# Kernel tuning notes

Measured on AMD Instinct MI355X. Metric: run time of the kernel, lower is better.

The kernel has to match this reference:

```python
import jax, jax.numpy as jnp
import numpy as np

B, N, E, S, ANN_D, N_STEPS = 16384, 70, 3, 10, 1, 5


def setup_inputs() -> dict:
    key = jax.random.key(0)
    ks = jax.random.split(key, 10)
    std = 0.02
    annotation = jax.random.normal(ks[0], (B, N), jnp.float32)
    A_raw = jax.random.uniform(ks[1], (N, N * E), jnp.float32) + 1e-3
    A = A_raw / A_raw.sum(axis=1, keepdims=True)  # row-normalized like torch.div(A, sum(A,1))
    W_in = jax.random.normal(ks[2], (E, S, S), jnp.float32) * std
    b_in = jnp.zeros((E, S), jnp.float32)
    Wr = jax.random.normal(ks[3], (S, 2 * S), jnp.float32) * std
    br = jnp.zeros((S,), jnp.float32)
    Wz = jax.random.normal(ks[4], (S, 2 * S), jnp.float32) * std
    bz = jnp.zeros((S,), jnp.float32)
    Wh = jax.random.normal(ks[5], (S, 2 * S), jnp.float32) * std
    bh = jnp.zeros((S,), jnp.float32)
    Wo1 = jax.random.normal(ks[6], (S, S + ANN_D), jnp.float32) * std
    bo1 = jnp.zeros((S,), jnp.float32)
    Wo2 = jax.random.normal(ks[7], (1, S), jnp.float32) * std
    bo2 = jnp.zeros((1,), jnp.float32)
    return {"annotation": annotation, "A": A, "W_in": W_in, "b_in": b_in,
            "Wr": Wr, "br": br, "Wz": Wz, "bz": bz, "Wh": Wh, "bh": bh,
            "Wo1": Wo1, "bo1": bo1, "Wo2": Wo2, "bo2": bo2}


def reference(annotation, A, W_in, b_in, Wr, br, Wz, bz, Wh, bh, Wo1, bo1, Wo2, bo2):
    b, n = annotation.shape
    ann = annotation[..., None]  # [B, N, 1]
    # initial state: annotation padded with zeros to state_dim
    prop = jnp.concatenate([ann, jnp.zeros((b, n, S - ANN_D), annotation.dtype)], axis=2)  # [B,N,S]
    for _ in range(N_STEPS):
        # per-edge-type linear: [B,E,N,S]; view order is edge-type-major (matches torch stack/transpose/view)
        ins = jnp.einsum('bnd,efd->benf', prop, W_in) + b_in[None, :, None, :]
        ins = ins.reshape(b, E * n, S)  # [B, E*N, S]
        a_in = jnp.einsum('nm,bms->bns', A, ins)  # bmm aggregation, [B,N,S]
        a = jnp.concatenate([a_in, prop], axis=2)  # [B,N,2S]
        r = jax.nn.sigmoid(a @ Wr.T + br)
        z = jax.nn.sigmoid(a @ Wz.T + bz)
        joined = jnp.concatenate([a_in, r * prop], axis=2)
        h_hat = jnp.tanh(joined @ Wh.T + bh)
        prop = (1.0 - z) * prop + z * h_hat
    join_state = jnp.concatenate([prop, ann], axis=2)  # [B,N,S+1]
    out = jnp.tanh(join_state @ Wo1.T + bo1) @ Wo2.T + bo2  # [B,N,1]
    return out.sum(axis=2)  # [B,N]
```

## Files before the change

### kernel.cpp

```cpp
#include <hip/hip_runtime.h>
#include <hip/hip_bf16.h>

typedef _Float16 v8h __attribute__((ext_vector_type(8)));
typedef _Float16 v4h __attribute__((ext_vector_type(4)));
typedef _Float16 v2h __attribute__((ext_vector_type(2)));
typedef float    v4f __attribute__((ext_vector_type(4)));
typedef int      v4i __attribute__((ext_vector_type(4)));
typedef int      v2i __attribute__((ext_vector_type(2)));

#define NTOT  16384
#define NN    70
#define STEPS 5
#define TPB   64
#define NBLK  NTOT
#define CATN  40
#define CATH  3208
#define USTR  232
#define UH    (10*USTR)

#define PWO1 0
#define PWO2 120
#define PBO2 130
#define NWP  132

#define OFR  1024
#define OFZ  1536
#define OFH  2048
#define OFA  2560
#define NWF  20480
#define PREPB 40

__device__ __align__(16) float    g_w[NWP];
__device__ __align__(16) _Float16 g_wf[NWF];
__device__ int g_flag;

__device__ __forceinline__ float fast_sigmoid(float x) {
    return __builtin_amdgcn_rcpf(1.0f + __expf(-x));
}
__device__ __forceinline__ float fast_tanh(float x) {
    float ax = fabsf(x);
    float e  = __expf(-2.0f * ax);
    float t  = (1.0f - e) * __builtin_amdgcn_rcpf(1.0f + e);
    return copysignf(t, x);
}
__device__ __forceinline__ v4h pk4(v4f a) {
    auto lo = __builtin_amdgcn_cvt_pkrtz(a[0], a[1]);
    auto hi = __builtin_amdgcn_cvt_pkrtz(a[2], a[3]);
    v4h r; r[0] = lo[0]; r[1] = lo[1]; r[2] = hi[0]; r[3] = hi[1];
    return r;
}

struct __align__(16) Smem {
    _Float16 U[UH];
    _Float16 cat[CATH];
};

__global__ void prep_kernel(const void* annv, const void* Av,
    const void* winv, const void* binv, const void* wrv, const void* brv,
    const void* wzv, const void* bzv, const void* whv, const void* bhv,
    const void* wo1v, const void* bo1v, const void* wo2v, const void* bo2v)
{
    __shared__ int sflag;
    if (threadIdx.x == 0) {
        const unsigned short* u = (const unsigned short*)annv;
        int good = 0;
        for (int k = 0; k < 128; ++k) {
            unsigned short bb = u[k];
            int ex = (bb >> 7) & 0xFF;
            if (bb == 0 || (ex >= 101 && ex <= 131)) ++good;
        }
        sflag = (good >= 112) ? 1 : 0;
        if (blockIdx.x == 0) g_flag = sflag;
    }
    __syncthreads();
    const int f = sflag;
    #define RD(p, i) (f ? (float)((const __hip_bfloat16*)(p))[i] : ((const float*)(p))[i])
    const int tid = threadIdx.x;
    if (blockIdx.x == 0) {
        for (int idx = tid; idx < 120; idx += blockDim.x) {
            const int s = idx / 12, cc = idx - s*12;
            g_w[PWO1 + idx] = (cc < 11) ? RD(wo1v, s*11 + cc) : RD(bo1v, s);
        }
        for (int idx = tid; idx < 10; idx += blockDim.x) g_w[PWO2 + idx] = RD(wo2v, idx);
        if (tid == 0) { g_w[PBO2] = RD(bo2v, 0); g_w[PBO2+1] = 0.f; }
    }
    for (int idx = blockIdx.x*blockDim.x + tid; idx < NWF; idx += gridDim.x*blockDim.x) {
        float val = 0.f;
        if (idx < OFR) {
            const int nt = idx >> 9, rem = idx & 511, lane = rem >> 3, j = rem & 7;
            const int k = ((lane >> 4) << 3) + j, col = nt*16 + (lane & 15);
            if (col < 30) {
                const int e = col / 10, s = col - e*10;
                if (k >= 16 && k < 26) val = RD(winv, e*100 + s*10 + (k-16));
                else if (k == 26)      val = RD(binv, e*10 + s);
            }
        } else if (idx < OFH) {
            const int i2 = idx - OFR;
            const int mt = i2 >> 9, rem = i2 & 511, lane = rem >> 3, j = rem & 7;
            const int k = ((lane >> 4) << 3) + j, s = lane & 15;
            if (s < 10) {
                const void* Wv = mt ? wzv : wrv;
                const void* bv = mt ? bzv : brv;
                if (k < 10)                 val = RD(Wv, s*20 + k);
                else if (k >= 16 && k < 26) val = RD(Wv, s*20 + 10 + (k-16));
                else if (k == 26)           val = RD(bv, s);
            }
        } else if (idx < OFA) {
            const int i2 = idx - OFH;
            const int lane = i2 >> 3, j = i2 & 7;
            const int k = ((lane >> 4) << 3) + j, s = lane & 15;
            if (s < 10) {
                if (k < 10)                 val = RD(whv, s*20 + k);
                else if (k >= 16 && k < 26) val = RD(whv, s*20 + 10 + (k-16));
                else if (k == 26)           val = RD(bhv, s);
            }
        } else {
            const int i2 = idx - OFA;
            const int w = i2 / 3584, rem = i2 - w*3584;
            const int kt = rem >> 9, r2 = rem & 511, lane = r2 >> 3, j = r2 & 7;
            const int m = w*16 + (lane & 15);
            const int k = kt*32 + ((lane >> 4) << 3) + j;
            const int e = k / 72, mm = k - e*72;
            if (m < NN && e < 3 && mm < NN) val = RD(Av, m*210 + e*70 + mm);
        }
        g_wf[idx] = (_Float16)val;
    }
    #undef RD
}

template<typename T>
__device__ __forceinline__ void run_impl(const void* annv, void* outv, Smem& sm)
{
    const T* ann_g = (const T*)annv;
    T* out_g       = (T*)outv;
    const int lane = threadIdx.x;
    const int blk  = blockIdx.x;
    const int q    = lane >> 4;
    const int c    = lane & 15;
    const float* __restrict__ gw = g_w;

    const v8h w1f0 = *(const v8h*)&g_wf[       lane*8];
    const v8h w1f1 = *(const v8h*)&g_wf[512  + lane*8];
    const v8h wrf  = *(const v8h*)&g_wf[OFR  + lane*8];
    const v8h wzf  = *(const v8h*)&g_wf[OFZ  + lane*8];
    const v8h whf  = *(const v8h*)&g_wf[OFH  + lane*8];
    v8h adj[35];
    #pragma unroll
    for (int i = 0; i < 35; ++i)
        adj[i] = *(const v8h*)&g_wf[OFA + i*512 + lane*8];

    const int a_lo  = c << 2;
    const int a_mid = (16 + c) << 2;
    const int a_sel = (q == 3) ? ((32 + c) << 2) : a_lo;

    {
        const int4 zz = {0,0,0,0};
        int4* z = (int4*)&sm;
        #pragma unroll 4
        for (int i = lane; i < (int)(sizeof(Smem)/16); i += TPB) z[i] = zz;
    }
    __syncthreads();

    for (int n2 = lane; n2 < NN; n2 += TPB) {
        sm.cat[n2*CATN + 16] = (_Float16)(float)ann_g[blk*NN + n2];
        sm.cat[n2*CATN + 26] = (_Float16)1.0f;
    }
    __syncthreads();

    #define PHASE1() do {                                                        \
        _Pragma("unroll")                                                        \
        for (int mt = 0; mt < 5; ++mt) {                                         \
            const v8h af = *(const v8h*)&sm.cat[(mt*16 + c)*CATN + q*8];         \
            const int node0 = mt*16 + q*4;                                       \
            _Pragma("unroll")                                                    \
            for (int nt = 0; nt < 2; ++nt) {                                     \
                v4f acc = {0.f,0.f,0.f,0.f};                                     \
                acc = __builtin_amdgcn_mfma_f32_16x16x32_f16(                    \
                        af, nt ? w1f1 : w1f0, acc, 0,0,0);                       \
                const int colw = nt*16 + c;                                      \
                if (colw < 30 && node0 <= 68) {                                  \
                    const int e = colw / 10, s = colw - e*10;                    \
                    *(v4h*)&sm.U[s*USTR + e*72 + node0] = pk4(acc);              \
                }                                                                \
            }                                                                    \
        }                                                                        \
    } while(0)

    PHASE1();
    __syncthreads();

    #pragma unroll 1
    for (int step = 0; step < STEPS; ++step) {
        {
            v8h bfr[7];
            #pragma unroll
            for (int kt = 0; kt < 7; ++kt)
                bfr[kt] = *(const v8h*)&sm.U[c*USTR + q*8 + kt*32];
            #pragma unroll
            for (int mt = 0; mt < 5; ++mt) {
                v4f acc = {0.f,0.f,0.f,0.f};
                #pragma unroll
                for (int kt = 0; kt < 7; ++kt)
                    acc = __builtin_amdgcn_mfma_f32_16x16x32_f16(
                        bfr[kt], adj[mt*7+kt], acc, 0,0,0);
                const int node = mt*16 + c;
                if (node < NN) {
                    const v4h hv = pk4(acc);
                    _Float16* wp = &sm.cat[node*CATN + q*4];
                    if (q < 2)       *(v4h*)wp = hv;
                    else if (q == 2) *(v2h*)wp = (v2h){hv[0], hv[1]};
                }
            }
        }
        __syncthreads();

        {
            #pragma unroll
            for (int nt = 0; nt < 5; ++nt) {
                const int node = nt*16 + c;
                const v8h bf = *(const v8h*)&sm.cat[node*CATN + q*8];
                v4f ar = {0.f,0.f,0.f,0.f}, az = {0.f,0.f,0.f,0.f};
                ar = __builtin_amdgcn_mfma_f32_16x16x32_f16(wrf, bf, ar, 0,0,0);
                az = __builtin_amdgcn_mfma_f32_16x16x32_f16(wzf, bf, az, 0,0,0);
                const v4h pv = *(const v4h*)&sm.cat[node*CATN + 16 + q*4];
                float pg[4], zg[4];
                v4f rpf;
                #pragma unroll
                for (int i = 0; i < 4; ++i) {
                    pg[i]  = (float)pv[i];
                    zg[i]  = fast_sigmoid(az[i]);
                    rpf[i] = fast_sigmoid(ar[i]) * pg[i];
                }
                const v4h rp = pk4(rpf);
                const v2i rpi = __builtin_bit_cast(v2i, rp);
                const int d0 = __builtin_amdgcn_ds_bpermute(a_sel, rpi[0]);
                const int d1 = __builtin_amdgcn_ds_bpermute(a_lo,  rpi[1]);
                const int d2 = __builtin_amdgcn_ds_bpermute(a_mid, rpi[0]);
                const int d3 = __builtin_amdgcn_ds_bpermute(a_mid, rpi[1]);
                const v4i bfi = __builtin_bit_cast(v4i, bf);
                v4i b2;
                b2[0] = (q < 2) ? bfi[0] : d0;
                b2[1] = (q < 2) ? bfi[1] : ((q == 2) ? d1 : 0x00003C00);
                b2[2] = (q < 2) ? bfi[2] : ((q == 2) ? d2 : 0);
                b2[3] = (q < 2) ? bfi[3] : ((q == 2) ? d3 : 0);
                const v8h bf2 = __builtin_bit_cast(v8h, b2);
                v4f ah = {0.f,0.f,0.f,0.f};
                ah = __builtin_amdgcn_mfma_f32_16x16x32_f16(whf, bf2, ah, 0,0,0);
                v4h pn;
                #pragma unroll
                for (int i = 0; i < 4; ++i) {
                    const float hh = fast_tanh(ah[i]);
                    pn[i] = (_Float16)(pg[i] + zg[i]*(hh - pg[i]));
                }
                if (node < NN) {
                    _Float16* wp = &sm.cat[node*CATN + 16 + q*4];
                    if (q < 2)       *(v4h*)wp = pn;
                    else if (q == 2) *(v2h*)wp = (v2h){pn[0], pn[1]};
                }
            }
        }
        __syncthreads();

        if (step < STEPS-1) {
            PHASE1();
            __syncthreads();
        }
    }
    #undef PHASE1

    for (int n2 = lane; n2 < NN; n2 += TPB) {
        const _Float16* pc = &sm.cat[n2*CATN + 16];
        const v8h p8 = *(const v8h*)pc;
        const v2h p2 = *(const v2h*)(pc + 8);
        float pr[10];
        #pragma unroll
        for (int i = 0; i < 8; ++i) pr[i] = (float)p8[i];
        pr[8] = (float)p2[0]; pr[9] = (float)p2[1];
        const float av = (float)ann_g[blk*NN + n2];
        float o = gw[PBO2];
        #pragma unroll
        for (int s = 0; s < 10; ++s) {
            const float* wr_ = &gw[PWO1 + s*12];
            float acc = wr_[11] + wr_[10]*av;
            #pragma unroll
            for (int d = 0; d < 10; ++d) acc += pr[d]*wr_[d];
            o += fast_tanh(acc) * gw[PWO2 + s];
        }
        out_g[blk*NN + n2] = (T)o;
    }
}

__global__ __launch_bounds__(TPB, 2)
void ggnn_kernel(const void* annv, void* outv)
{
    __shared__ Smem sm;
    if (g_flag)
        run_impl<__hip_bfloat16>(annv, outv, sm);
    else
        run_impl<float>(annv, outv, sm);
}

extern "C" void kernel_launch(void* const* d_in, const int* in_sizes, int n_in,
                              void* d_out, int out_size, void* d_ws, size_t ws_size,
                              hipStream_t stream) {
    (void)in_sizes; (void)n_in; (void)out_size; (void)d_ws; (void)ws_size;
    hipLaunchKernelGGL(prep_kernel, dim3(PREPB), dim3(256), 0, stream,
        d_in[0], d_in[1], d_in[2], d_in[3], d_in[4], d_in[5], d_in[6],
        d_in[7], d_in[8], d_in[9], d_in[10], d_in[11], d_in[12], d_in[13]);
    hipLaunchKernelGGL(ggnn_kernel, dim3(NBLK), dim3(TPB), 0, stream,
        d_in[0], d_out);
}
```

Baseline: 259.2 us.

## Fuse next-step edge projection into GRU update via cross-lane permutes

```diff
diff --git a/kernel.cpp b/kernel.cpp
--- a/kernel.cpp
+++ b/kernel.cpp
@@ -167,26 +167,24 @@
     }
     __syncthreads();
 
-    #define PHASE1() do {                                                        \
-        _Pragma("unroll")                                                        \
-        for (int mt = 0; mt < 5; ++mt) {                                         \
-            const v8h af = *(const v8h*)&sm.cat[(mt*16 + c)*CATN + q*8];         \
-            const int node0 = mt*16 + q*4;                                       \
-            _Pragma("unroll")                                                    \
-            for (int nt = 0; nt < 2; ++nt) {                                     \
-                v4f acc = {0.f,0.f,0.f,0.f};                                     \
-                acc = __builtin_amdgcn_mfma_f32_16x16x32_f16(                    \
-                        af, nt ? w1f1 : w1f0, acc, 0,0,0);                       \
-                const int colw = nt*16 + c;                                      \
-                if (colw < 30 && node0 <= 68) {                                  \
-                    const int e = colw / 10, s = colw - e*10;                    \
-                    *(v4h*)&sm.U[s*USTR + e*72 + node0] = pk4(acc);              \
-                }                                                                \
-            }                                                                    \
-        }                                                                        \
-    } while(0)
-
-    PHASE1();
+    {
+        #pragma unroll
+        for (int mt = 0; mt < 5; ++mt) {
+            const v8h af = *(const v8h*)&sm.cat[(mt*16 + c)*CATN + q*8];
+            const int node0 = mt*16 + q*4;
+            #pragma unroll
+            for (int nt = 0; nt < 2; ++nt) {
+                v4f acc = {0.f,0.f,0.f,0.f};
+                acc = __builtin_amdgcn_mfma_f32_16x16x32_f16(
+                        af, nt ? w1f1 : w1f0, acc, 0,0,0);
+                const int colw = nt*16 + c;
+                if (colw < 30 && node0 <= 68) {
+                    const int e = colw / 10, s = colw - e*10;
+                    *(v4h*)&sm.U[s*USTR + e*72 + node0] = pk4(acc);
+                }
+            }
+        }
+    }
     __syncthreads();
 
     #pragma unroll 1
@@ -257,16 +255,35 @@
                     if (q < 2)       *(v4h*)wp = pn;
                     else if (q == 2) *(v2h*)wp = (v2h){pn[0], pn[1]};
                 }
+                if (step < STEPS-1) {
+                    const v2i pni = __builtin_bit_cast(v2i, pn);
+                    const int e0 = __builtin_amdgcn_ds_bpermute(a_sel, pni[0]);
+                    const int e1 = __builtin_amdgcn_ds_bpermute(a_lo,  pni[1]);
+                    const int e2 = __builtin_amdgcn_ds_bpermute(a_mid, pni[0]);
+                    const int e3 = __builtin_amdgcn_ds_bpermute(a_mid, pni[1]);
+                    v4i afi;
+                    afi[0] = (q < 2) ? 0 : e0;
+                    afi[1] = (q < 2) ? 0 : ((q == 2) ? e1 : 0x00003C00);
+                    afi[2] = (q == 2) ? e2 : 0;
+                    afi[3] = (q == 2) ? e3 : 0;
+                    const v8h af = __builtin_bit_cast(v8h, afi);
+                    const int node0 = nt*16 + q*4;
+                    #pragma unroll
+                    for (int nt2 = 0; nt2 < 2; ++nt2) {
+                        v4f acc = {0.f,0.f,0.f,0.f};
+                        acc = __builtin_amdgcn_mfma_f32_16x16x32_f16(
+                                af, nt2 ? w1f1 : w1f0, acc, 0,0,0);
+                        const int colw = nt2*16 + c;
+                        if (colw < 30 && node0 <= 68) {
+                            const int e = colw / 10, s = colw - e*10;
+                            *(v4h*)&sm.U[s*USTR + e*72 + node0] = pk4(acc);
+                        }
+                    }
+                }
             }
         }
         __syncthreads();
-
-        if (step < STEPS-1) {
-            PHASE1();
-            __syncthreads();
-        }
-    }
-    #undef PHASE1
+    }
 
     for (int n2 = lane; n2 < NN; n2 += TPB) {
         const _Float16* pc = &sm.cat[n2*CATN + 16];
```

New measurement: 262.7 us. No clear change (+1.4%).
